# Kernel optimization log

Hardware: AMD Instinct MI355X
Metric: run time of the kernel (lower is better)

## Reference

```python
import jax, jax.numpy as jnp
import numpy as np

B = 4096      # batch of omics samples
IN = 4096     # input_dim (genes)
NP = 512      # num_pathways (df_comp columns)
DP1 = 8       # dim_per_path_1
DP2 = 16      # dim_per_path_2
P1 = NP * DP1 # 4096
P2 = NP * DP2 # 8192
H = P2 // 4   # 2048 hidden of to_logits
NC = 4        # num_classes


def _xavier(k, shape):
    return jax.random.normal(k, shape, jnp.float32) * jnp.sqrt(2.0 / (shape[0] + shape[1]))


def setup_inputs() -> dict:
    key = jax.random.key(0)
    ks = jax.random.split(key, 10)
    return {
        "x_omic": jax.random.normal(ks[0], (B, IN), jnp.float32),
        "fc1_w": _xavier(ks[1], (IN, P1)),
        "fc1_b": jax.random.uniform(ks[2], (P1,), jnp.float32),
        "fc2_w": _xavier(ks[3], (P1, P2)),
        "fc2_b": jax.random.uniform(ks[4], (P2,), jnp.float32),
        "w1": _xavier(ks[5], (P2, H)),
        "b1": jax.random.uniform(ks[6], (H,), jnp.float32),
        "w2": _xavier(ks[7], (H, NC)),
        "b2": jax.random.uniform(ks[8], (NC,), jnp.float32),
        # binary pathway-membership matrix (df_comp.values)
        "comp": jax.random.randint(ks[9], (IN, NP), 0, 2, dtype=jnp.int32),
    }


def reference(x_omic, fc1_w, fc1_b, fc2_w, fc2_b, w1, b1, w2, b2, comp):
    dt = fc1_w.dtype
    # mask_1: each pathway membership column expanded to dim_per_path_1 columns
    mask1 = jnp.repeat(comp.astype(dt), DP1, axis=1)                 # [IN, P1]
    mask2 = jnp.kron(jnp.eye(NP, dtype=dt), jnp.ones((DP1, DP2), dt))  # [P1, P2]

    out = x_omic @ (fc1_w * mask1) + fc1_b      # [B, P1]
    out = out @ (fc2_w * mask2) + fc2_b         # [B, P2]
    # to_logits MLP (dropout is identity in eval)
    h = jax.nn.relu(out @ w1 + b1)              # [B, H]
    logits = (h @ w2 + b2)[None]                # [1, B, NC] (unsqueeze(0))
    Y_hat = jnp.argmax(logits, axis=1, keepdims=True)  # topk(k=1, dim=1) indices
    hazards = jax.nn.sigmoid(logits)
    S = jnp.cumprod(1.0 - hazards, axis=1)
    return hazards, S, Y_hat
```

## Files before the change

kernel.cpp:

```cpp
#include <hip/hip_runtime.h>
#include <cmath>

typedef _Float16 h8  __attribute__((ext_vector_type(8)));
typedef _Float16 h4v __attribute__((ext_vector_type(4)));
typedef float    f4  __attribute__((ext_vector_type(4)));

#define NB  4096
#define NIN 4096
#define NNP 512
#define NP1 4096
#define NP2 8192
#define NH  2048

__device__ __forceinline__ void g2l(const void* g, void* l) {
  __builtin_amdgcn_global_load_lds((const __attribute__((address_space(1))) void*)g,
                                   (__attribute__((address_space(3))) void*)l, 16, 0, 0);
}

__global__ __launch_bounds__(256) void k_pack_f16(const float* __restrict__ in,
                                                  _Float16* __restrict__ out, int n4) {
  int i = blockIdx.x * 256 + threadIdx.x;
  if (i >= n4) return;
  f4 v = ((const f4*)in)[i];
  h4v o;
  o[0] = (_Float16)v[0]; o[1] = (_Float16)v[1];
  o[2] = (_Float16)v[2]; o[3] = (_Float16)v[3];
  ((h4v*)out)[i] = o;
}

template<bool MASK>
__global__ __launch_bounds__(256) void k_packT(const float* __restrict__ in,
                                               const int* __restrict__ comp,
                                               _Float16* __restrict__ out, int K, int N) {
  __shared__ float tile[64][65];
  const int n0 = blockIdx.x * 64, k0 = blockIdx.y * 64;
  const int tx = threadIdx.x & 63, ty = threadIdx.x >> 6;
#pragma unroll
  for (int r = 0; r < 16; ++r) {
    int kk = r * 4 + ty;
    float v = in[(long)(k0 + kk) * N + n0 + tx];
    if (MASK) v *= (float)comp[(long)(k0 + kk) * NNP + ((n0 + tx) >> 3)];
    tile[kk][tx] = v;
  }
  __syncthreads();
#pragma unroll
  for (int r = 0; r < 16; ++r) {
    int nn = r * 4 + ty;
    out[(long)(n0 + nn) * K + k0 + tx] = (_Float16)tile[tx][nn];
  }
}

template<int EPI>
__global__ __launch_bounds__(512, 1) void k_gemm8(
    const _Float16* __restrict__ A, const _Float16* __restrict__ BT,
    const float* __restrict__ bias, _Float16* __restrict__ C,
    int M, int N, int K, int nbn, int ksplit) {
  extern __shared__ char smem[];
  const int nwg = gridDim.x;
  const int q = nwg >> 3, r = nwg & 7;
  const int xcd = blockIdx.x & 7, idx = blockIdx.x >> 3;
  const int wg = (xcd < r ? xcd * (q + 1) : r * (q + 1) + (xcd - r) * q) + idx;
  const int tpk = nwg / ksplit;
  const int ks = wg / tpk;
  const int rem = wg - ks * tpk;
  const int bm = rem / nbn, bn = rem % nbn;
  const long m0 = (long)bm << 8, n0 = (long)bn << 8;
  const int Ks = K / ksplit;
  const int NT = Ks >> 6;

  const int tid = threadIdx.x;
  const int lane = tid & 63, w = tid >> 6;
  const int wm = w >> 2, wn = w & 3;
  const int lh = lane & 15, ls = lane >> 4;
  const int swz = (lh & 7) << 4;
  const int c0 = (ls * 16) ^ swz;
  const int c1 = (64 + ls * 16) ^ swz;
  const int arow = (wm * 64 + lh) * 128;
  const int brow = 32768 + (wn * 32 + lh) * 128;

  const long sKb = (long)K * 2;
  const int scb = (((tid & 7) ^ ((tid >> 3) & 7)) << 4);
  const char* Ag = (const char*)A + (m0 + (tid >> 3)) * sKb + (long)ks * Ks * 2 + scb;
  const char* Bg = (const char*)BT + (n0 + (tid >> 3)) * sKb + (long)ks * Ks * 2 + scb;
  const long h64 = 64 * sKb, h128 = 128 * sKb;
  const int lw = w << 10;

#define STAGE_A(buf, hh, kb) do { \
    const char* s_ = Ag + (hh) * h128 + (kb); \
    char* d_ = smem + (buf) * 65536 + (hh) * 16384 + lw; \
    g2l(s_, d_); g2l(s_ + h64, d_ + 8192); } while (0)
#define STAGE_B(buf, hh, kb) do { \
    const char* s_ = Bg + (hh) * h128 + (kb); \
    char* d_ = smem + (buf) * 65536 + 32768 + (hh) * 16384 + lw; \
    g2l(s_, d_); g2l(s_ + h64, d_ + 8192); } while (0)
#define READ_A(dst, buf, mh) do { \
    _Pragma("unroll") for (int m_ = 0; m_ < 4; ++m_) { \
      dst[m_][0] = *(const h8*)(smem + (buf) * 65536 + (mh) * 16384 + arow + m_ * 2048 + c0); \
      dst[m_][1] = *(const h8*)(smem + (buf) * 65536 + (mh) * 16384 + arow + m_ * 2048 + c1); } } while (0)
#define READ_B(dst, buf, nh) do { \
    _Pragma("unroll") for (int n_ = 0; n_ < 2; ++n_) { \
      dst[n_][0] = *(const h8*)(smem + (buf) * 65536 + (nh) * 16384 + brow + n_ * 2048 + c0); \
      dst[n_][1] = *(const h8*)(smem + (buf) * 65536 + (nh) * 16384 + brow + n_ * 2048 + c1); } } while (0)
#define MM(mh, nh, aset, bset) do { \
    _Pragma("unroll") for (int kq_ = 0; kq_ < 2; ++kq_) \
    _Pragma("unroll") for (int m_ = 0; m_ < 4; ++m_) \
    _Pragma("unroll") for (int n_ = 0; n_ < 2; ++n_) \
      acc[mh][nh][m_][n_] = __builtin_amdgcn_mfma_f32_16x16x32_f16(aset[m_][kq_], bset[n_][kq_], acc[mh][nh][m_][n_], 0, 0, 0); } while (0)
#define BAR() asm volatile("s_barrier" ::: "memory")
#define VM6() asm volatile("s_waitcnt vmcnt(6)" ::: "memory")
#define VM8() asm volatile("s_waitcnt vmcnt(8)" ::: "memory")
#define PR1() __builtin_amdgcn_s_setprio(1)
#define PR0() __builtin_amdgcn_s_setprio(0)

  f4 acc[2][2][4][2] = {};
  h8 afA[4][2], afB[4][2];
  h8 bfA[2][2], bfB[2][2];

  auto kc = [&](int t) -> long { return (long)(t < NT ? t : NT - 1) << 7; };

  STAGE_A(0, 0, kc(0)); STAGE_B(0, 0, kc(0)); STAGE_B(0, 1, kc(0)); STAGE_A(0, 1, kc(0));
  STAGE_A(1, 0, kc(1)); STAGE_B(1, 0, kc(1)); STAGE_B(1, 1, kc(1)); STAGE_A(1, 1, kc(1));
  VM8();
  BAR();
  READ_A(afA, 0, 0);
  READ_B(bfA, 0, 0);

  for (int t2 = 0; t2 < NT; t2 += 2) {
    BAR();
    READ_B(bfB, 0, 1);
    STAGE_A(0, 0, kc(t2 + 2));
    PR1(); MM(0, 0, afA, bfA); PR0();
    BAR();
    READ_A(afB, 0, 1);
    STAGE_B(0, 1, kc(t2 + 2));
    PR1(); MM(0, 1, afA, bfB); PR0();
    BAR();
    STAGE_A(0, 1, kc(t2 + 2));
    VM6();
    READ_A(afA, 1, 0);
    PR1(); MM(1, 1, afB, bfB); PR0();
    BAR();
    READ_B(bfB, 1, 0);
    STAGE_B(0, 0, kc(t2 + 2));
    PR1(); MM(1, 0, afB, bfA); PR0();
    BAR();
    READ_B(bfA, 1, 1);
    STAGE_A(1, 0, kc(t2 + 3));
    PR1(); MM(0, 0, afA, bfB); PR0();
    BAR();
    READ_A(afB, 1, 1);
    STAGE_B(1, 1, kc(t2 + 3));
    PR1(); MM(0, 1, afA, bfA); PR0();
    BAR();
    STAGE_A(1, 1, kc(t2 + 3));
    VM6();
    READ_A(afA, 0, 0);
    PR1(); MM(1, 1, afB, bfA); PR0();
    BAR();
    READ_B(bfA, 0, 0);
    STAGE_B(1, 0, kc(t2 + 3));
    PR1(); MM(1, 0, afB, bfB); PR0();
  }

  _Float16* dst = (EPI == 1) ? (C + (long)ks * M * N) : C;
#pragma unroll
  for (int mh = 0; mh < 2; ++mh)
#pragma unroll
  for (int m = 0; m < 4; ++m) {
    const long r0 = m0 + mh * 128 + wm * 64 + m * 16 + ls * 4;
#pragma unroll
    for (int nh = 0; nh < 2; ++nh)
#pragma unroll
    for (int n = 0; n < 2; ++n) {
      const long c = n0 + nh * 128 + wn * 32 + n * 16 + lh;
      const float bv = (EPI == 0) ? bias[c] : 0.f;
#pragma unroll
      for (int j = 0; j < 4; ++j)
        dst[(r0 + j) * N + c] = (_Float16)(acc[mh][nh][m][n][j] + bv);
    }
  }
#undef STAGE_A
#undef STAGE_B
#undef READ_A
#undef READ_B
#undef MM
#undef BAR
#undef VM6
#undef VM8
#undef PR1
#undef PR0
}

__global__ __launch_bounds__(256) void k_gemm2(const _Float16* __restrict__ out1,
                                               const float* __restrict__ fc2w,
                                               const float* __restrict__ fc2b,
                                               _Float16* __restrict__ out2) {
  const int b0 = (blockIdx.x >> 4) * 64;
  const int p  = (blockIdx.x & 15) * 32 + (threadIdx.x & 31);
  const int bsub = threadIdx.x >> 5;
  f4 bb0 = *(const f4*)&fc2b[p * 16 + 0];
  f4 bb1 = *(const f4*)&fc2b[p * 16 + 4];
  f4 bb2 = *(const f4*)&fc2b[p * 16 + 8];
  f4 bb3 = *(const f4*)&fc2b[p * 16 + 12];
  for (int r = 0; r < 8; ++r) {
    const int b = b0 + r * 8 + bsub;
    h8 qv = *(const h8*)&out1[(long)b * NP1 + p * 8];
    f4 a0 = bb0, a1 = bb1, a2 = bb2, a3 = bb3;
#pragma unroll
    for (int i = 0; i < 8; ++i) {
      const float qi = (float)qv[i];
      const f4* wr = (const f4*)&fc2w[(long)(p * 8 + i) * NP2 + p * 16];
      a0 += qi * wr[0]; a1 += qi * wr[1]; a2 += qi * wr[2]; a3 += qi * wr[3];
    }
    h8 o0, o1;
#pragma unroll
    for (int u = 0; u < 4; ++u) {
      o0[u] = (_Float16)a0[u]; o0[4 + u] = (_Float16)a1[u];
      o1[u] = (_Float16)a2[u]; o1[4 + u] = (_Float16)a3[u];
    }
    h8* dstp = (h8*)&out2[(long)b * NP2 + p * 16];
    dstp[0] = o0; dstp[1] = o1;
  }
}

__global__ __launch_bounds__(256) void k_logits(const _Float16* __restrict__ part,
                                                const float* __restrict__ b1,
                                                const float* __restrict__ w2,
                                                const float* __restrict__ b2,
                                                float* __restrict__ logits,
                                                float* __restrict__ hazards) {
  const int lane = threadIdx.x & 63;
  const int b = blockIdx.x * 4 + (threadIdx.x >> 6);
  const long off2 = (long)NB * NH;
  f4 acc = {0.f, 0.f, 0.f, 0.f};
  const _Float16* p0 = part + (long)b * NH;
  const _Float16* p1 = p0 + off2;
#pragma unroll
  for (int c4 = 0; c4 < 4; ++c4) {
    const int k0 = c4 * 512 + lane * 8;
    h8 a = *(const h8*)&p0[k0];
    h8 bb = *(const h8*)&p1[k0];
    f4 bva = *(const f4*)&b1[k0];
    f4 bvb = *(const f4*)&b1[k0 + 4];
#pragma unroll
    for (int u = 0; u < 8; ++u) {
      const float bias = (u < 4) ? bva[u] : bvb[u - 4];
      const float hv = fmaxf((float)a[u] + (float)bb[u] + bias, 0.f);
      acc += hv * *(const f4*)&w2[(long)(k0 + u) * 4];
    }
  }
#pragma unroll
  for (int off = 32; off > 0; off >>= 1) {
#pragma unroll
    for (int u = 0; u < 4; ++u) acc[u] += __shfl_xor(acc[u], off, 64);
  }
  if (lane == 0) {
    f4 lg = acc + *(const f4*)b2;
    ((f4*)logits)[b] = lg;
    f4 hz;
#pragma unroll
    for (int u = 0; u < 4; ++u) hz[u] = 1.f / (1.f + expf(-lg[u]));
    ((f4*)hazards)[b] = hz;
  }
}

__global__ __launch_bounds__(256) void k_final(const float* __restrict__ logits,
                                               const float* __restrict__ hazards,
                                               float* __restrict__ S,
                                               float* __restrict__ yhat) {
  const int c = blockIdx.x;
  const int t = threadIdx.x;
  __shared__ float pl[256];
  __shared__ float mv[256];
  __shared__ int   mi[256];
  float prod = 1.f;
  float best = -1e30f; int bi = 0;
  for (int i = 0; i < 16; ++i) {
    const int b = t * 16 + i;
    prod *= (1.f - hazards[b * 4 + c]);
    const float lg = logits[b * 4 + c];
    if (lg > best) { best = lg; bi = b; }
  }
  pl[t] = prod; mv[t] = best; mi[t] = bi;
  __syncthreads();
  for (int off = 1; off < 256; off <<= 1) {
    float cur  = pl[t];
    float prev = (t >= off) ? pl[t - off] : 1.f;
    __syncthreads();
    pl[t] = cur * prev;
    __syncthreads();
  }
  float s = (t == 0) ? 1.f : pl[t - 1];
  for (int i = 0; i < 16; ++i) {
    const int b = t * 16 + i;
    s *= (1.f - hazards[b * 4 + c]);
    S[b * 4 + c] = s;
  }
  for (int off = 128; off > 0; off >>= 1) {
    if (t < off) {
      float ov = mv[t + off]; int oi = mi[t + off];
      if (ov > mv[t] || (ov == mv[t] && oi < mi[t])) { mv[t] = ov; mi[t] = oi; }
    }
    __syncthreads();
  }
  if (t == 0) yhat[c] = (float)mi[0];
}

extern "C" void kernel_launch(void* const* d_in, const int* in_sizes, int n_in,
                              void* d_out, int out_size, void* d_ws, size_t ws_size,
                              hipStream_t stream) {
  (void)in_sizes; (void)n_in; (void)out_size; (void)ws_size;
  const float* x    = (const float*)d_in[0];
  const float* fc1w = (const float*)d_in[1];
  const float* fc1b = (const float*)d_in[2];
  const float* fc2w = (const float*)d_in[3];
  const float* fc2b = (const float*)d_in[4];
  const float* w1   = (const float*)d_in[5];
  const float* b1   = (const float*)d_in[6];
  const float* w2   = (const float*)d_in[7];
  const float* b2   = (const float*)d_in[8];
  const int*   comp = (const int*)d_in[9];

  char* ws = (char*)d_ws;
  const size_t MB = 1024ull * 1024ull;
  _Float16* xh     = (_Float16*)(ws + 0);
  _Float16* w1mT   = (_Float16*)(ws + 32 * MB);
  _Float16* out1h  = (_Float16*)(ws + 64 * MB);
  _Float16* out2h  = (_Float16*)(ws + 96 * MB);
  _Float16* w1Th   = (_Float16*)(ws + 0);
  _Float16* part   = (_Float16*)(ws + 32 * MB);
  float*    logits = (float*)(ws + 64 * MB);
  float*    outF   = (float*)d_out;

  hipFuncSetAttribute(reinterpret_cast<const void*>(k_gemm8<0>),
                      hipFuncAttributeMaxDynamicSharedMemorySize, 131072);
  hipFuncSetAttribute(reinterpret_cast<const void*>(k_gemm8<1>),
                      hipFuncAttributeMaxDynamicSharedMemorySize, 131072);

  k_pack_f16<<<(NB * NIN / 4) / 256, 256, 0, stream>>>(x, xh, NB * NIN / 4);
  k_packT<true><<<dim3(NP1 / 64, NIN / 64), 256, 0, stream>>>(fc1w, comp, w1mT, NIN, NP1);
  k_gemm8<0><<<(NB / 256) * (NP1 / 256), 512, 131072, stream>>>(
      xh, w1mT, fc1b, out1h, NB, NP1, NIN, NP1 / 256, 1);
  k_gemm2<<<(NB / 64) * (NNP / 32), 256, 0, stream>>>(out1h, fc2w, fc2b, out2h);
  k_packT<false><<<dim3(NH / 64, NP2 / 64), 256, 0, stream>>>(w1, nullptr, w1Th, NP2, NH);
  k_gemm8<1><<<(NB / 256) * (NH / 256) * 2, 512, 131072, stream>>>(
      out2h, w1Th, nullptr, part, NB, NH, NP2, NH / 256, 2);
  k_logits<<<NB / 4, 256, 0, stream>>>(part, b1, w2, b2, logits, outF);
  k_final<<<4, 256, 0, stream>>>(logits, outF, outF + NB * 4, outF + 2 * NB * 4);
}
```

Before: 336.8 us.

## Fold block-diagonal fc2 into w1 to shrink the to_logits GEMM K dimension

```diff
diff --git a/kernel.cpp b/kernel.cpp
--- a/kernel.cpp
+++ b/kernel.cpp
@@ -48,6 +48,55 @@
     int nn = r * 4 + ty;
     out[(long)(n0 + nn) * K + k0 + tx] = (_Float16)tile[tx][nn];
   }
+}
+
+__global__ __launch_bounds__(256) void k_wc(const float* __restrict__ fc2w,
+                                            const float* __restrict__ w1,
+                                            const float* __restrict__ fc2b,
+                                            _Float16* __restrict__ WcT,
+                                            float* __restrict__ partialB) {
+  const int p = blockIdx.x;
+  const int tid = threadIdx.x;
+  __shared__ float fs[8][16];
+  __shared__ float bs[16];
+  if (tid < 128) {
+    int i = tid >> 4, jj = tid & 15;
+    fs[i][jj] = fc2w[(long)(p * 8 + i) * NP2 + p * 16 + jj];
+  }
+  if (tid < 16) bs[tid] = fc2b[p * 16 + tid];
+  __syncthreads();
+#pragma unroll
+  for (int c = 0; c < 8; ++c) {
+    const int j = c * 256 + tid;
+    float acc[8] = {0.f, 0.f, 0.f, 0.f, 0.f, 0.f, 0.f, 0.f};
+    float bacc = 0.f;
+#pragma unroll
+    for (int jj = 0; jj < 16; ++jj) {
+      const float w1v = w1[(long)(p * 16 + jj) * NH + j];
+      bacc += bs[jj] * w1v;
+#pragma unroll
+      for (int i = 0; i < 8; ++i) acc[i] += fs[i][jj] * w1v;
+    }
+    h8 o;
+#pragma unroll
+    for (int i = 0; i < 8; ++i) o[i] = (_Float16)acc[i];
+    *(h8*)&WcT[(long)j * NP1 + p * 8] = o;
+    partialB[(long)p * NH + j] = bacc;
+  }
+}
+
+__global__ __launch_bounds__(256) void k_bias2(const float* __restrict__ partialB,
+                                               const float* __restrict__ b1,
+                                               float* __restrict__ biasc) {
+  const int j = blockIdx.x * 256 + threadIdx.x;
+  float a0 = 0.f, a1 = 0.f, a2 = 0.f, a3 = 0.f;
+  for (int p = 0; p < NNP; p += 4) {
+    a0 += partialB[(long)p * NH + j];
+    a1 += partialB[(long)(p + 1) * NH + j];
+    a2 += partialB[(long)(p + 2) * NH + j];
+    a3 += partialB[(long)(p + 3) * NH + j];
+  }
+  biasc[j] = a0 + a1 + a2 + a3 + b1[j];
 }
 
 template<int EPI>
@@ -191,38 +240,6 @@
 #undef PR0
 }
 
-__global__ __launch_bounds__(256) void k_gemm2(const _Float16* __restrict__ out1,
-                                               const float* __restrict__ fc2w,
-                                               const float* __restrict__ fc2b,
-                                               _Float16* __restrict__ out2) {
-  const int b0 = (blockIdx.x >> 4) * 64;
-  const int p  = (blockIdx.x & 15) * 32 + (threadIdx.x & 31);
-  const int bsub = threadIdx.x >> 5;
-  f4 bb0 = *(const f4*)&fc2b[p * 16 + 0];
-  f4 bb1 = *(const f4*)&fc2b[p * 16 + 4];
-  f4 bb2 = *(const f4*)&fc2b[p * 16 + 8];
-  f4 bb3 = *(const f4*)&fc2b[p * 16 + 12];
-  for (int r = 0; r < 8; ++r) {
-    const int b = b0 + r * 8 + bsub;
-    h8 qv = *(const h8*)&out1[(long)b * NP1 + p * 8];
-    f4 a0 = bb0, a1 = bb1, a2 = bb2, a3 = bb3;
-#pragma unroll
-    for (int i = 0; i < 8; ++i) {
-      const float qi = (float)qv[i];
-      const f4* wr = (const f4*)&fc2w[(long)(p * 8 + i) * NP2 + p * 16];
-      a0 += qi * wr[0]; a1 += qi * wr[1]; a2 += qi * wr[2]; a3 += qi * wr[3];
-    }
-    h8 o0, o1;
-#pragma unroll
-    for (int u = 0; u < 4; ++u) {
-      o0[u] = (_Float16)a0[u]; o0[4 + u] = (_Float16)a1[u];
-      o1[u] = (_Float16)a2[u]; o1[4 + u] = (_Float16)a3[u];
-    }
-    h8* dstp = (h8*)&out2[(long)b * NP2 + p * 16];
-    dstp[0] = o0; dstp[1] = o1;
-  }
-}
-
 __global__ __launch_bounds__(256) void k_logits(const _Float16* __restrict__ part,
                                                 const float* __restrict__ b1,
                                                 const float* __restrict__ w2,
@@ -326,8 +343,9 @@
   _Float16* xh     = (_Float16*)(ws + 0);
   _Float16* w1mT   = (_Float16*)(ws + 32 * MB);
   _Float16* out1h  = (_Float16*)(ws + 64 * MB);
-  _Float16* out2h  = (_Float16*)(ws + 96 * MB);
-  _Float16* w1Th   = (_Float16*)(ws + 0);
+  _Float16* WcT    = (_Float16*)(ws + 96 * MB);
+  float*    partB  = (float*)(ws + 112 * MB);
+  float*    biasc  = (float*)(ws + 116 * MB);
   _Float16* part   = (_Float16*)(ws + 32 * MB);
   float*    logits = (float*)(ws + 64 * MB);
   float*    outF   = (float*)d_out;
@@ -339,12 +357,12 @@
 
   k_pack_f16<<<(NB * NIN / 4) / 256, 256, 0, stream>>>(x, xh, NB * NIN / 4);
   k_packT<true><<<dim3(NP1 / 64, NIN / 64), 256, 0, stream>>>(fc1w, comp, w1mT, NIN, NP1);
+  k_wc<<<NNP, 256, 0, stream>>>(fc2w, w1, fc2b, WcT, partB);
+  k_bias2<<<NH / 256, 256, 0, stream>>>(partB, b1, biasc);
   k_gemm8<0><<<(NB / 256) * (NP1 / 256), 512, 131072, stream>>>(
       xh, w1mT, fc1b, out1h, NB, NP1, NIN, NP1 / 256, 1);
-  k_gemm2<<<(NB / 64) * (NNP / 32), 256, 0, stream>>>(out1h, fc2w, fc2b, out2h);
-  k_packT<false><<<dim3(NH / 64, NP2 / 64), 256, 0, stream>>>(w1, nullptr, w1Th, NP2, NH);
   k_gemm8<1><<<(NB / 256) * (NH / 256) * 2, 512, 131072, stream>>>(
-      out2h, w1Th, nullptr, part, NB, NH, NP2, NH / 256, 2);
-  k_logits<<<NB / 4, 256, 0, stream>>>(part, b1, w2, b2, logits, outF);
+      out1h, WcT, nullptr, part, NB, NH, NP1, NH / 256, 2);
+  k_logits<<<NB / 4, 256, 0, stream>>>(part, biasc, w2, b2, logits, outF);
   k_final<<<4, 256, 0, stream>>>(logits, outF, outF + NB * 4, outF + 2 * NB * 4);
 }
```

After: 381.9 us. 13.4% more time.
